# Kernel tuning notes

Hardware: AMD Instinct MI355X
Metric: run time of the kernel (lower is better)

The kernel has to match this reference:

```python
import jax, jax.numpy as jnp
import numpy as np
import math

DIM = 2048
B, Q_LEN, KV_LEN = 8, 128, 4096


def setup_inputs() -> dict:
    key = jax.random.key(0)
    ks = jax.random.split(key, 8)
    x = jax.random.normal(ks[0], (B, Q_LEN, DIM), dtype=jnp.float32)
    mask = jnp.zeros((B, Q_LEN, KV_LEN + Q_LEN), dtype=bool)  # unused by the original forward
    k_cache = jax.random.normal(ks[1], (B, KV_LEN, DIM), dtype=jnp.float32)
    v_cache = jax.random.normal(ks[2], (B, KV_LEN, DIM), dtype=jnp.float32)
    scale = 1.0 / math.sqrt(DIM)
    wq = jax.random.normal(ks[3], (DIM, DIM), dtype=jnp.float32) * scale
    wk = jax.random.normal(ks[4], (DIM, DIM), dtype=jnp.float32) * scale
    wv = jax.random.normal(ks[5], (DIM, DIM), dtype=jnp.float32) * scale
    wo = jax.random.normal(ks[6], (DIM, DIM), dtype=jnp.float32) * scale
    return {"x": x, "mask": mask, "k_cache": k_cache, "v_cache": v_cache,
            "wq": wq, "wk": wk, "wv": wv, "wo": wo}


def reference(x, mask, k_cache, v_cache, wq, wk, wv, wo):
    # Linear layers (torch: y = x @ W^T)
    q = jnp.einsum('bsd,ed->bse', x, wq)
    k_new = jnp.einsum('bsd,ed->bse', x, wk)
    v_new = jnp.einsum('bsd,ed->bse', x, wv)
    # KV-cache growth via concat (the pattern the kernel replaces)
    k = jnp.concatenate([k_cache, k_new], axis=1)  # [B, KV+Q, D]
    v = jnp.concatenate([v_cache, v_new], axis=1)
    scale = 1.0 / math.sqrt(q.shape[-1])
    scores = jnp.einsum('bqd,bkd->bqk', q, k) * scale  # [B, Q, KV+Q]
    attn = jax.nn.softmax(scores, axis=-1)             # NOTE: mask is unused, as in original
    out = jnp.einsum('bqk,bkd->bqd', attn, v)
    return jnp.einsum('bqd,ed->bqe', out, wo)
```

## Files before the change

### kernel.cpp

```cpp
#include <hip/hip_runtime.h>

typedef __bf16 bf16;
typedef __bf16 bf16x4 __attribute__((ext_vector_type(4)));
typedef __bf16 bf16x8 __attribute__((ext_vector_type(8)));
typedef float f32x4 __attribute__((ext_vector_type(4)));

#define DIM   2048
#define BQ    128
#define KVL   4096
#define KVT   4224
#define SCALE 0.022097086912079608f

__device__ __forceinline__ int swz(int row, int col) {
  return row * 64 + (col ^ ((row & 7) << 3));
}

template<int R, int NTHR>
struct PBg {
  static constexpr int N8 = R * 64 / (NTHR * 8);
  bf16x8 v[N8];
  __device__ __forceinline__ void load(const bf16* __restrict__ src, int ld, int tid) {
    const int r0 = tid >> 3, c = (tid & 7) * 8;
    #pragma unroll
    for (int j = 0; j < N8; ++j)
      v[j] = *reinterpret_cast<const bf16x8*>(src + (size_t)(j * (NTHR / 8) + r0) * ld + c);
  }
  __device__ __forceinline__ void write(bf16* dst, int tid) {
    const int r0 = tid >> 3, c = (tid & 7) * 8;
    #pragma unroll
    for (int j = 0; j < N8; ++j)
      *reinterpret_cast<bf16x8*>(dst + swz(j * (NTHR / 8) + r0, c)) = v[j];
  }
};

struct PU64 {
  float4 v[4];
  int r0, c;
  __device__ __forceinline__ void init(int tid) { r0 = tid >> 4; c = (tid & 15) * 4; }
  __device__ __forceinline__ void loadF(const float* __restrict__ src, int ld) {
    #pragma unroll
    for (int j = 0; j < 4; ++j)
      v[j] = *reinterpret_cast<const float4*>(src + (size_t)(j * 16 + r0) * ld + c);
  }
  __device__ __forceinline__ void loadB(const bf16* __restrict__ src, int ld) {
    #pragma unroll
    for (int j = 0; j < 4; ++j) {
      bf16x4 t = *reinterpret_cast<const bf16x4*>(src + (size_t)(j * 16 + r0) * ld + c);
      v[j].x = (float)t[0]; v[j].y = (float)t[1]; v[j].z = (float)t[2]; v[j].w = (float)t[3];
    }
  }
  __device__ __forceinline__ void write(bf16* dst) {
    #pragma unroll
    for (int j = 0; j < 4; ++j) {
      bf16x4 b;
      b[0] = (bf16)v[j].x; b[1] = (bf16)v[j].y; b[2] = (bf16)v[j].z; b[3] = (bf16)v[j].w;
      *reinterpret_cast<bf16x4*>(dst + swz(j * 16 + r0, c)) = b;
    }
  }
};

struct PVT {
  float v[16];
  int vn, vk0;
  __device__ __forceinline__ void init(int tid) { vn = tid & 63; vk0 = (tid >> 6) * 16; }
  __device__ __forceinline__ void loadF(const float* __restrict__ src) {
    #pragma unroll
    for (int i = 0; i < 16; ++i) v[i] = src[(size_t)(vk0 + i) * DIM + vn];
  }
  __device__ __forceinline__ void loadB(const bf16* __restrict__ src) {
    #pragma unroll
    for (int i = 0; i < 16; ++i) v[i] = (float)src[(size_t)(vk0 + i) * DIM + vn];
  }
  __device__ __forceinline__ void write(bf16* dst) {
    #pragma unroll
    for (int j = 0; j < 4; ++j) {
      bf16x4 t;
      #pragma unroll
      for (int i = 0; i < 4; ++i) t[i] = (bf16)v[4 * j + i];
      *reinterpret_cast<bf16x4*>(dst + swz(vn, vk0 + 4 * j)) = t;
    }
  }
};

template<int MF, int NF>
__device__ __forceinline__ void mma_tile(const bf16* As, const bf16* Bs,
                                         f32x4 (&acc)[MF][NF], int l, int wm, int wn) {
  const int ar = l & 15;
  const int ak = (l >> 4) * 8;
  bf16x8 a[MF][2], b[NF][2];
  #pragma unroll
  for (int mi = 0; mi < MF; ++mi)
    #pragma unroll
    for (int kk = 0; kk < 2; ++kk)
      a[mi][kk] = *reinterpret_cast<const bf16x8*>(As + swz(wm + mi * 16 + ar, kk * 32 + ak));
  #pragma unroll
  for (int ni = 0; ni < NF; ++ni)
    #pragma unroll
    for (int kk = 0; kk < 2; ++kk)
      b[ni][kk] = *reinterpret_cast<const bf16x8*>(Bs + swz(wn + ni * 16 + ar, kk * 32 + ak));
  #pragma unroll
  for (int kk = 0; kk < 2; ++kk)
    #pragma unroll
    for (int mi = 0; mi < MF; ++mi)
      #pragma unroll
      for (int ni = 0; ni < NF; ++ni)
        acc[mi][ni] = __builtin_amdgcn_mfma_f32_16x16x32_bf16(
            a[mi][kk], b[ni][kk], acc[mi][ni], 0, 0, 0);
}

__global__ __launch_bounds__(256) void k_cvt(const float* __restrict__ x,
    const float* __restrict__ wq, const float* __restrict__ wk,
    const float* __restrict__ wv, const float* __restrict__ wo,
    bf16* __restrict__ xb, bf16* __restrict__ wb) {
  const int seg = blockIdx.y;
  const float* src; bf16* dst; int n; float sc = 1.0f;
  if (seg == 0)      { src = x;  dst = xb;            n = 1024 * DIM; }
  else if (seg == 1) { src = wq; dst = wb;            n = DIM * DIM; sc = SCALE; }
  else if (seg == 2) { src = wk; dst = wb + 1 * DIM * DIM; n = DIM * DIM; }
  else if (seg == 3) { src = wv; dst = wb + 2 * DIM * DIM; n = DIM * DIM; }
  else               { src = wo; dst = wb + 3 * DIM * DIM; n = DIM * DIM; }
  const int i0 = (blockIdx.x * 256 + threadIdx.x) * 8;
  if (i0 >= n) return;
  #pragma unroll
  for (int h = 0; h < 2; ++h) {
    float4 v = *reinterpret_cast<const float4*>(src + i0 + 4 * h);
    bf16x4 b;
    b[0] = (bf16)(v.x * sc); b[1] = (bf16)(v.y * sc);
    b[2] = (bf16)(v.z * sc); b[3] = (bf16)(v.w * sc);
    *reinterpret_cast<bf16x4*>(dst + i0 + 4 * h) = b;
  }
}

__global__ __launch_bounds__(256) void k_qkv(const bf16* __restrict__ xb,
    const bf16* __restrict__ wb,
    bf16* __restrict__ qb, bf16* __restrict__ kb, bf16* __restrict__ vb) {
  __shared__ bf16 As[2][128 * 64];
  __shared__ bf16 Bs[2][64 * 64];
  const int nt = blockIdx.x;
  const int w  = nt >> 5;
  const int col0 = (nt & 31) * 64;
  bf16* __restrict__ O = (w == 0) ? qb : (w == 1) ? kb : vb;
  const int m0 = blockIdx.y * 128;
  const int tid = threadIdx.x, l = tid & 63, wid = tid >> 6;
  const int wm = (wid >> 1) * 64, wn = (wid & 1) * 32;
  const bf16* Ap = xb + (size_t)m0 * DIM;
  const bf16* Bp = wb + (size_t)nt * 64 * DIM;
  PBg<128, 256> pa; PBg<64, 256> pb;
  f32x4 acc[4][2] = {};
  pa.load(Ap, DIM, tid); pb.load(Bp, DIM, tid);
  pa.write(As[0], tid);  pb.write(Bs[0], tid);
  int cur = 0;
  constexpr int NT = DIM / 64;
  for (int kt = 0; kt < NT; ++kt) {
    if (kt + 1 < NT) { pa.load(Ap + (kt + 1) * 64, DIM, tid); pb.load(Bp + (kt + 1) * 64, DIM, tid); }
    __syncthreads();
    mma_tile<4, 2>(As[cur], Bs[cur], acc, l, wm, wn);
    if (kt + 1 < NT) { pa.write(As[cur ^ 1], tid); pb.write(Bs[cur ^ 1], tid); }
    cur ^= 1;
  }
  const int rr = (l >> 4) * 4, cc = l & 15;
  #pragma unroll
  for (int mi = 0; mi < 4; ++mi)
    #pragma unroll
    for (int ni = 0; ni < 2; ++ni)
      #pragma unroll
      for (int r = 0; r < 4; ++r)
        O[(size_t)(m0 + wm + mi * 16 + rr + r) * DIM + col0 + wn + ni * 16 + cc] =
            (bf16)acc[mi][ni][r];
}

__global__ __launch_bounds__(256) void k_scores(const bf16* __restrict__ qb,
    const bf16* __restrict__ kb, const float* __restrict__ kcache,
    float* __restrict__ scores) {
  __shared__ bf16 As[2][128 * 64];
  __shared__ bf16 Bs[2][64 * 64];
  const int nt = blockIdx.x;
  const int b  = blockIdx.y;
  const int tid = threadIdx.x, l = tid & 63, wid = tid >> 6;
  const int wm = (wid >> 1) * 64, wn = (wid & 1) * 32;
  const bf16* Q = qb + (size_t)b * BQ * DIM;
  const bool useCache = (nt < 64);
  const float* Bf = kcache + ((size_t)b * KVL + nt * 64) * DIM;
  const bf16*  Bb = kb + ((size_t)b * BQ + (nt - 64) * 64) * DIM;
  PBg<128, 256> pa; PU64 pu; pu.init(tid);
  f32x4 acc[4][2] = {};
  pa.load(Q, DIM, tid);
  if (useCache) pu.loadF(Bf, DIM); else pu.loadB(Bb, DIM);
  pa.write(As[0], tid); pu.write(Bs[0]);
  int cur = 0;
  constexpr int NT = DIM / 64;
  for (int kt = 0; kt < NT; ++kt) {
    if (kt + 1 < NT) {
      pa.load(Q + (kt + 1) * 64, DIM, tid);
      if (useCache) pu.loadF(Bf + (kt + 1) * 64, DIM); else pu.loadB(Bb + (kt + 1) * 64, DIM);
    }
    __syncthreads();
    mma_tile<4, 2>(As[cur], Bs[cur], acc, l, wm, wn);
    if (kt + 1 < NT) { pa.write(As[cur ^ 1], tid); pu.write(Bs[cur ^ 1]); }
    cur ^= 1;
  }
  const int rr = (l >> 4) * 4, cc = l & 15;
  #pragma unroll
  for (int mi = 0; mi < 4; ++mi)
    #pragma unroll
    for (int ni = 0; ni < 2; ++ni)
      #pragma unroll
      for (int r = 0; r < 4; ++r)
        scores[((size_t)b * BQ + wm + mi * 16 + rr + r) * KVT + nt * 64 + wn + ni * 16 + cc] =
            acc[mi][ni][r];
}

__global__ __launch_bounds__(256) void k_softmax(const float* __restrict__ scores,
                                                 bf16* __restrict__ attn) {
  __shared__ float s[KVT];
  __shared__ float red[4];
  const int row = blockIdx.x;
  const int tid = threadIdx.x;
  const size_t base = (size_t)row * KVT;
  float ls = 0.f;
  for (int i = tid * 4; i < KVT; i += 1024) {
    float4 v = *reinterpret_cast<const float4*>(scores + base + i);
    float e0 = __expf(v.x), e1 = __expf(v.y), e2 = __expf(v.z), e3 = __expf(v.w);
    *reinterpret_cast<float4*>(s + i) = make_float4(e0, e1, e2, e3);
    ls += (e0 + e1) + (e2 + e3);
  }
  #pragma unroll
  for (int off = 32; off >= 1; off >>= 1) ls += __shfl_xor(ls, off, 64);
  if ((tid & 63) == 0) red[tid >> 6] = ls;
  __syncthreads();
  const float inv = 1.f / ((red[0] + red[1]) + (red[2] + red[3]));
  for (int i = tid * 4; i < KVT; i += 1024) {
    float4 e = *reinterpret_cast<const float4*>(s + i);
    bf16x4 o;
    o[0] = (bf16)(e.x * inv); o[1] = (bf16)(e.y * inv);
    o[2] = (bf16)(e.z * inv); o[3] = (bf16)(e.w * inv);
    *reinterpret_cast<bf16x4*>(attn + base + i) = o;
  }
}

__global__ __launch_bounds__(256) void k_pv(const bf16* __restrict__ attn,
    const float* __restrict__ vcache, const bf16* __restrict__ vb,
    float* __restrict__ pp) {
  __shared__ bf16 As[2][128 * 64];
  __shared__ bf16 VT[2][64 * 64];
  const int n0 = blockIdx.x * 64;
  const int b  = blockIdx.y;
  const int c  = blockIdx.z;
  const int tid = threadIdx.x, l = tid & 63, wid = tid >> 6;
  const int wm = (wid >> 1) * 64, wn = (wid & 1) * 32;
  const bf16* Ap = attn + (size_t)b * BQ * KVT + c * 2112;
  PBg<128, 256> pa; PVT pv; pv.init(tid);
  f32x4 acc[4][2] = {};
  auto loadV = [&](int lk) {
    const int grow = c * 2112 + lk * 64;
    if (grow < KVL) pv.loadF(vcache + ((size_t)b * KVL + grow) * DIM + n0);
    else            pv.loadB(vb + ((size_t)b * BQ + (grow - KVL)) * DIM + n0);
  };
  pa.load(Ap, KVT, tid); loadV(0);
  pa.write(As[0], tid);  pv.write(VT[0]);
  int cur = 0;
  constexpr int NT = 33;
  for (int kt = 0; kt < NT; ++kt) {
    if (kt + 1 < NT) { pa.load(Ap + (kt + 1) * 64, KVT, tid); loadV(kt + 1); }
    __syncthreads();
    mma_tile<4, 2>(As[cur], VT[cur], acc, l, wm, wn);
    if (kt + 1 < NT) { pa.write(As[cur ^ 1], tid); pv.write(VT[cur ^ 1]); }
    cur ^= 1;
  }
  float* P = pp + (size_t)c * 1024 * DIM;
  const int rr = (l >> 4) * 4, cc = l & 15;
  #pragma unroll
  for (int mi = 0; mi < 4; ++mi)
    #pragma unroll
    for (int ni = 0; ni < 2; ++ni)
      #pragma unroll
      for (int r = 0; r < 4; ++r)
        P[((size_t)b * BQ + wm + mi * 16 + rr + r) * DIM + n0 + wn + ni * 16 + cc] =
            acc[mi][ni][r];
}

__global__ __launch_bounds__(256) void k_pvcomb(const float* __restrict__ pp,
                                                bf16* __restrict__ ob) {
  const int i0 = (blockIdx.x * 256 + threadIdx.x) * 4;
  float4 a = *reinterpret_cast<const float4*>(pp + i0);
  float4 b = *reinterpret_cast<const float4*>(pp + 1024 * DIM + i0);
  bf16x4 o;
  o[0] = (bf16)(a.x + b.x); o[1] = (bf16)(a.y + b.y);
  o[2] = (bf16)(a.z + b.z); o[3] = (bf16)(a.w + b.w);
  *reinterpret_cast<bf16x4*>(ob + i0) = o;
}

__global__ __launch_bounds__(256) void k_oproj(const bf16* __restrict__ ob,
    const bf16* __restrict__ wob, float* __restrict__ out) {
  __shared__ bf16 As[2][128 * 64];
  __shared__ bf16 Bs[2][64 * 64];
  const int n0 = blockIdx.x * 64;
  const int m0 = blockIdx.y * 128;
  const int tid = threadIdx.x, l = tid & 63, wid = tid >> 6;
  const int wm = (wid >> 1) * 64, wn = (wid & 1) * 32;
  const bf16* Ap = ob  + (size_t)m0 * DIM;
  const bf16* Bp = wob + (size_t)n0 * DIM;
  PBg<128, 256> pa; PBg<64, 256> pb;
  f32x4 acc[4][2] = {};
  pa.load(Ap, DIM, tid); pb.load(Bp, DIM, tid);
  pa.write(As[0], tid);  pb.write(Bs[0], tid);
  int cur = 0;
  constexpr int NT = DIM / 64;
  for (int kt = 0; kt < NT; ++kt) {
    if (kt + 1 < NT) { pa.load(Ap + (kt + 1) * 64, DIM, tid); pb.load(Bp + (kt + 1) * 64, DIM, tid); }
    __syncthreads();
    mma_tile<4, 2>(As[cur], Bs[cur], acc, l, wm, wn);
    if (kt + 1 < NT) { pa.write(As[cur ^ 1], tid); pb.write(Bs[cur ^ 1], tid); }
    cur ^= 1;
  }
  const int rr = (l >> 4) * 4, cc = l & 15;
  #pragma unroll
  for (int mi = 0; mi < 4; ++mi)
    #pragma unroll
    for (int ni = 0; ni < 2; ++ni)
      #pragma unroll
      for (int r = 0; r < 4; ++r)
        out[(size_t)(m0 + wm + mi * 16 + rr + r) * DIM + n0 + wn + ni * 16 + cc] =
            acc[mi][ni][r];
}

extern "C" void kernel_launch(void* const* d_in, const int* in_sizes, int n_in,
                              void* d_out, int out_size, void* d_ws, size_t ws_size,
                              hipStream_t stream) {
  const float* x      = (const float*)d_in[0];
  const float* kcache = (const float*)d_in[2];
  const float* vcache = (const float*)d_in[3];
  const float* wq     = (const float*)d_in[4];
  const float* wk     = (const float*)d_in[5];
  const float* wv     = (const float*)d_in[6];
  const float* wo     = (const float*)d_in[7];
  float* out = (float*)d_out;

  char* ws = (char*)d_ws;
  bf16*  xb     = (bf16*)(ws + 0);
  bf16*  wb     = (bf16*)(ws + 4194304);
  bf16*  qb     = (bf16*)(ws + 37748736);
  bf16*  kb     = (bf16*)(ws + 41943040);
  bf16*  vb     = (bf16*)(ws + 46137344);
  float* scores = (float*)(ws + 50331648);
  bf16*  attnb  = (bf16*)(ws + 67633152);
  bf16*  obuf   = (bf16*)(ws + 76283904);
  float* pp     = (float*)(ws + 80478208);
  bf16*  wob    = wb + (size_t)3 * DIM * DIM;

  k_cvt<<<dim3(2048, 5), 256, 0, stream>>>(x, wq, wk, wv, wo, xb, wb);
  k_qkv<<<dim3(96, 8), 256, 0, stream>>>(xb, wb, qb, kb, vb);
  k_scores<<<dim3(66, 8), 256, 0, stream>>>(qb, kb, kcache, scores);
  k_softmax<<<dim3(1024), 256, 0, stream>>>(scores, attnb);
  k_pv<<<dim3(32, 8, 2), 256, 0, stream>>>(attnb, vcache, vb, pp);
  k_pvcomb<<<dim3(2048), 256, 0, stream>>>(pp, obuf);
  k_oproj<<<dim3(32, 8), 256, 0, stream>>>(obuf, wob, out);
}
```

Before: 244.8 us.

## Fuse exp into score GEMM epilogue and defer softmax normalization to PV combine

The score kernel now applies exp in its epilogue, writes unnormalized bf16 exponentials, and reduces per-row partial sums into a small buffer. A tiny kernel turns the partial sums into per-row inverses, and the PV combine kernel scales by them. This drops the fp32 score round-trip and the separate softmax pass. In exchange the epilogue does shuffle and shared-memory atomic reductions, adds a launch, and there is no max subtraction, so it relies on scores being small enough not to overflow.

```diff
diff --git a/kernel.cpp b/kernel.cpp
--- a/kernel.cpp
+++ b/kernel.cpp
@@ -171,9 +171,10 @@
 
 __global__ __launch_bounds__(256) void k_scores(const bf16* __restrict__ qb,
     const bf16* __restrict__ kb, const float* __restrict__ kcache,
-    float* __restrict__ scores) {
+    bf16* __restrict__ expb, float* __restrict__ partial) {
   __shared__ bf16 As[2][128 * 64];
   __shared__ bf16 Bs[2][64 * 64];
+  __shared__ float rs[128];
   const int nt = blockIdx.x;
   const int b  = blockIdx.y;
   const int tid = threadIdx.x, l = tid & 63, wid = tid >> 6;
@@ -199,43 +200,38 @@
     if (kt + 1 < NT) { pa.write(As[cur ^ 1], tid); pu.write(Bs[cur ^ 1]); }
     cur ^= 1;
   }
+  __syncthreads();
+  if (tid < 128) rs[tid] = 0.f;
+  __syncthreads();
   const int rr = (l >> 4) * 4, cc = l & 15;
   #pragma unroll
   for (int mi = 0; mi < 4; ++mi)
     #pragma unroll
-    for (int ni = 0; ni < 2; ++ni)
-      #pragma unroll
-      for (int r = 0; r < 4; ++r)
-        scores[((size_t)b * BQ + wm + mi * 16 + rr + r) * KVT + nt * 64 + wn + ni * 16 + cc] =
-            acc[mi][ni][r];
-}
-
-__global__ __launch_bounds__(256) void k_softmax(const float* __restrict__ scores,
-                                                 bf16* __restrict__ attn) {
-  __shared__ float s[KVT];
-  __shared__ float red[4];
-  const int row = blockIdx.x;
-  const int tid = threadIdx.x;
-  const size_t base = (size_t)row * KVT;
-  float ls = 0.f;
-  for (int i = tid * 4; i < KVT; i += 1024) {
-    float4 v = *reinterpret_cast<const float4*>(scores + base + i);
-    float e0 = __expf(v.x), e1 = __expf(v.y), e2 = __expf(v.z), e3 = __expf(v.w);
-    *reinterpret_cast<float4*>(s + i) = make_float4(e0, e1, e2, e3);
-    ls += (e0 + e1) + (e2 + e3);
-  }
-  #pragma unroll
-  for (int off = 32; off >= 1; off >>= 1) ls += __shfl_xor(ls, off, 64);
-  if ((tid & 63) == 0) red[tid >> 6] = ls;
+    for (int r = 0; r < 4; ++r) {
+      const float e0 = __expf(acc[mi][0][r]);
+      const float e1 = __expf(acc[mi][1][r]);
+      const int row = wm + mi * 16 + rr + r;
+      const size_t base = ((size_t)b * BQ + row) * KVT + nt * 64 + wn + cc;
+      expb[base]      = (bf16)e0;
+      expb[base + 16] = (bf16)e1;
+      float p = e0 + e1;
+      p += __shfl_xor(p, 1, 64);
+      p += __shfl_xor(p, 2, 64);
+      p += __shfl_xor(p, 4, 64);
+      p += __shfl_xor(p, 8, 64);
+      if ((l & 15) == 0) atomicAdd(&rs[row], p);
+    }
   __syncthreads();
-  const float inv = 1.f / ((red[0] + red[1]) + (red[2] + red[3]));
-  for (int i = tid * 4; i < KVT; i += 1024) {
-    float4 e = *reinterpret_cast<const float4*>(s + i);
-    bf16x4 o;
-    o[0] = (bf16)(e.x * inv); o[1] = (bf16)(e.y * inv);
-    o[2] = (bf16)(e.z * inv); o[3] = (bf16)(e.w * inv);
-    *reinterpret_cast<bf16x4*>(attn + base + i) = o;
-  }
+  if (tid < 128) partial[((size_t)b * BQ + tid) * 66 + nt] = rs[tid];
+}
+
+__global__ __launch_bounds__(256) void k_rowinv(const float* __restrict__ partial,
+                                                float* __restrict__ inv) {
+  const int row = blockIdx.x * 256 + threadIdx.x;
+  float s = 0.f;
+  #pragma unroll
+  for (int j = 0; j < 66; ++j) s += partial[(size_t)row * 66 + j];
+  inv[row] = 1.f / s;
 }
 
 __global__ __launch_bounds__(256) void k_pv(const bf16* __restrict__ attn,
@@ -280,13 +276,15 @@
 }
 
 __global__ __launch_bounds__(256) void k_pvcomb(const float* __restrict__ pp,
+                                                const float* __restrict__ inv,
                                                 bf16* __restrict__ ob) {
   const int i0 = (blockIdx.x * 256 + threadIdx.x) * 4;
+  const float iv = inv[i0 >> 11];
   float4 a = *reinterpret_cast<const float4*>(pp + i0);
   float4 b = *reinterpret_cast<const float4*>(pp + 1024 * DIM + i0);
   bf16x4 o;
-  o[0] = (bf16)(a.x + b.x); o[1] = (bf16)(a.y + b.y);
-  o[2] = (bf16)(a.z + b.z); o[3] = (bf16)(a.w + b.w);
+  o[0] = (bf16)((a.x + b.x) * iv); o[1] = (bf16)((a.y + b.y) * iv);
+  o[2] = (bf16)((a.z + b.z) * iv); o[3] = (bf16)((a.w + b.w) * iv);
   *reinterpret_cast<bf16x4*>(ob + i0) = o;
 }
 
@@ -337,22 +335,23 @@
   float* out = (float*)d_out;
 
   char* ws = (char*)d_ws;
-  bf16*  xb     = (bf16*)(ws + 0);
-  bf16*  wb     = (bf16*)(ws + 4194304);
-  bf16*  qb     = (bf16*)(ws + 37748736);
-  bf16*  kb     = (bf16*)(ws + 41943040);
-  bf16*  vb     = (bf16*)(ws + 46137344);
-  float* scores = (float*)(ws + 50331648);
-  bf16*  attnb  = (bf16*)(ws + 67633152);
-  bf16*  obuf   = (bf16*)(ws + 76283904);
-  float* pp     = (float*)(ws + 80478208);
-  bf16*  wob    = wb + (size_t)3 * DIM * DIM;
+  bf16*  xb      = (bf16*)(ws + 0);
+  bf16*  wb      = (bf16*)(ws + 4194304);
+  bf16*  qb      = (bf16*)(ws + 37748736);
+  bf16*  kb      = (bf16*)(ws + 41943040);
+  bf16*  vb      = (bf16*)(ws + 46137344);
+  float* partial = (float*)(ws + 50331648);
+  float* inv     = (float*)(ws + 50724864);
+  bf16*  expb    = (bf16*)(ws + 67633152);
+  bf16*  obuf    = (bf16*)(ws + 76283904);
+  float* pp      = (float*)(ws + 80478208);
+  bf16*  wob     = wb + (size_t)3 * DIM * DIM;
 
   k_cvt<<<dim3(2048, 5), 256, 0, stream>>>(x, wq, wk, wv, wo, xb, wb);
   k_qkv<<<dim3(96, 8), 256, 0, stream>>>(xb, wb, qb, kb, vb);
-  k_scores<<<dim3(66, 8), 256, 0, stream>>>(qb, kb, kcache, scores);
-  k_softmax<<<dim3(1024), 256, 0, stream>>>(scores, attnb);
-  k_pv<<<dim3(32, 8, 2), 256, 0, stream>>>(attnb, vcache, vb, pp);
-  k_pvcomb<<<dim3(2048), 256, 0, stream>>>(pp, obuf);
+  k_scores<<<dim3(66, 8), 256, 0, stream>>>(qb, kb, kcache, expb, partial);
+  k_rowinv<<<dim3(4), 256, 0, stream>>>(partial, inv);
+  k_pv<<<dim3(32, 8, 2), 256, 0, stream>>>(expb, vcache, vb, pp);
+  k_pvcomb<<<dim3(2048), 256, 0, stream>>>(pp, inv, obuf);
   k_oproj<<<dim3(32, 8), 256, 0, stream>>>(obuf, wob, out);
 }
```

Result: faster. 238.2 us, median of 2 (-2.7%).
